# Optimization experiments

Measured on AMD Instinct MI355X. Metric: run time of the kernel, lower is better.

Reference implementation:

```python
import jax, jax.numpy as jnp
import numpy as np

DT = 0.15
DX = 1.0
NUM_STEPS = 4
EPS = 1e-6


def smooth3(m, axis):
    # 3-tap mean filter with replicate padding (matches F.pad replicate + conv1d ones/3)
    pad = [(0, 0)] * m.ndim
    pad[axis] = (1, 1)
    p = jnp.pad(m, pad, mode='edge')
    n = m.shape[axis]
    s = lambda i: jax.lax.slice_in_dim(p, i, i + n, axis=axis)
    return (s(0) + s(1) + s(2)) / 3.0


def thomas(a, b, c, d):
    # a,b,c: [N, *S] coefficient diagonals; d: [N, *B] rhs, S broadcastable into B.
    # Single fused lax.scan per sweep instead of N python-level scatter steps.
    def fwd(carry, inp):
        cp, dp = carry
        ai, bi, ci, di = inp
        denom = bi - ai * cp + EPS  # first step: cp=0 -> b0 + eps, as in torch
        cn = ci / denom
        dn = (di - ai * dp) / denom
        return (cn, dn), (cn, dn)

    init = (jnp.zeros_like(b[0]), jnp.zeros_like(d[0]))
    _, (cs, ds) = jax.lax.scan(fwd, init, (a, b, c, d))
    cs = cs.at[-1].set(0.0)  # torch leaves c_star[N-1] = 0

    def bwd(xn, inp):
        ci, di = inp
        x = di - ci * xn
        return x, x

    _, xs = jax.lax.scan(bwd, jnp.zeros_like(ds[0]), (cs, ds), reverse=True)
    return xs  # [N, *B]


def _tridiag_coeffs(coeff_smooth, dt):
    coeff = coeff_smooth * dt / (DX ** 2)
    a = -coeff
    c = -coeff
    b = 1.0 + 2.0 * coeff
    b = b.at[..., 0].set(1.0 + coeff[..., 0])
    b = b.at[..., -1].set(1.0 + coeff[..., -1])
    return a, b, c


def diffuse_x(u, alpha, dt):
    # u: [B,C,H,W]; alpha: [C,H,W]; implicit solve along W
    asm = smooth3(alpha, axis=2)
    a, b, c = _tridiag_coeffs(asm, dt)  # [C,H,W], endpoints modified along W
    aT = jnp.moveaxis(a, -1, 0)  # [W,C,H]
    bT = jnp.moveaxis(b, -1, 0)
    cT = jnp.moveaxis(c, -1, 0)
    dT = jnp.moveaxis(u, -1, 0)  # [W,B,C,H]
    x = thomas(aT, bT, cT, dT)
    return jnp.moveaxis(x, 0, -1)


def diffuse_y(u, beta, dt):
    # u: [B,C,H,W]; beta: [C,H,W]; implicit solve along H
    bsm = smooth3(beta, axis=1)  # smoothing along H (torch smooths beta.T along last dim)
    coeff = bsm * dt / (DX ** 2)
    a = -coeff
    c = -coeff
    b = 1.0 + 2.0 * coeff
    b = b.at[:, 0, :].set(1.0 + coeff[:, 0, :])
    b = b.at[:, -1, :].set(1.0 + coeff[:, -1, :])
    aT = jnp.moveaxis(a, 1, 0)  # [H,C,W]
    bT = jnp.moveaxis(b, 1, 0)
    cT = jnp.moveaxis(c, 1, 0)
    dT = jnp.moveaxis(u, 2, 0)  # [H,B,C,W]
    x = thomas(aT, bT, cT, dT)
    return jnp.moveaxis(x, 0, 2)


def setup_inputs() -> dict:
    key = jax.random.key(0)
    ks = jax.random.split(key, 6)
    B, C, S = 16384, 3, 32
    u = jax.random.normal(ks[0], (B, C, S, S), dtype=jnp.float32)
    alpha_base = 1.2 + 0.05 * jax.random.normal(ks[1], (C, S, S), dtype=jnp.float32)
    beta_base = 1.2 + 0.05 * jax.random.normal(ks[2], (C, S, S), dtype=jnp.float32)
    alpha_time_coeff = 0.05 * jax.random.normal(ks[3], (C, S, S), dtype=jnp.float32)
    beta_time_coeff = 0.05 * jax.random.normal(ks[4], (C, S, S), dtype=jnp.float32)
    channel_coupling = 0.1 * jnp.eye(C, dtype=jnp.float32) + 0.01 * jax.random.normal(ks[5], (C, C), dtype=jnp.float32)
    return {"u": u, "alpha_base": alpha_base, "beta_base": beta_base,
            "alpha_time_coeff": alpha_time_coeff, "beta_time_coeff": beta_time_coeff,
            "channel_coupling": channel_coupling}


def reference(u, alpha_base, beta_base, alpha_time_coeff, beta_time_coeff, channel_coupling):
    t = 0.0
    for _ in range(NUM_STEPS):
        alpha = jnp.maximum(alpha_base + alpha_time_coeff * t, EPS)
        beta = jnp.maximum(beta_base + beta_time_coeff * t, EPS)
        u = diffuse_x(u, alpha, DT / 2)  # ADI half-step in x
        u = diffuse_y(u, beta, DT)       # full step in y
        u = diffuse_x(u, alpha, DT / 2)  # half-step in x
        # einsum 'cc,bci->bci' with repeated index = per-channel diagonal scaling
        u = jnp.einsum('cc,bchw->bchw', channel_coupling, u)
        t += DT
    return u
```

## Files before the change

kernel.cpp:

```cpp
#include <hip/hip_runtime.h>

#define EPS 1e-6f
#define NSTEPS 4
#define TPB 256
#define TILES 8
#define PITCH 33
#define TSTRIDE (32 * PITCH)

__global__ void coeff_kernel(const float* __restrict__ ab,
                             const float* __restrict__ atc,
                             const float* __restrict__ bb,
                             const float* __restrict__ btc,
                             float4* __restrict__ PX,
                             float4* __restrict__ PY)
{
    int tid = blockIdx.x * blockDim.x + threadIdx.x;
    if (tid >= 768) return;
    int lane = tid & 31;
    int rest = tid >> 5;
    int c    = rest % 3;
    int s    = (rest / 3) & 3;
    int dir  = rest / 12;
    float t  = 0.15f * (float)s;

    float A[32];
    float dt;
    if (dir == 0) {
        int h = lane;
        const float* pa = ab  + (c * 32 + h) * 32;
        const float* pt = atc + (c * 32 + h) * 32;
        #pragma unroll
        for (int w = 0; w < 32; w++)
            A[w] = fmaxf(pa[w] + t * pt[w], EPS);
        dt = 0.075f;
    } else {
        int w = lane;
        #pragma unroll
        for (int h = 0; h < 32; h++)
            A[h] = fmaxf(bb[(c * 32 + h) * 32 + w] + t * btc[(c * 32 + h) * 32 + w], EPS);
        dt = 0.15f;
    }

    float S[32];
    #pragma unroll
    for (int i = 0; i < 32; i++) {
        float l = A[(i == 0) ? 0 : i - 1];
        float r = A[(i == 31) ? 31 : i + 1];
        S[i] = (l + A[i] + r) / 3.0f;
    }

    float4* dst = (dir == 0 ? PX : PY) + ((s * 3 + c) * 32) * 32 + lane;
    float cp = 0.0f;
    for (int i = 0; i < 32; i++) {
        float co = S[i] * dt;
        float a  = -co;
        float b  = (i == 0 || i == 31) ? (1.0f + co) : (1.0f + 2.0f * co);
        float cc = -co;
        float denom = (b - a * cp) + EPS;
        float inv = 1.0f / denom;
        float cs  = cc / denom;
        if (i == 31) cs = 0.0f;
        dst[i * 32] = make_float4(a, inv, cs, 0.0f);
        cp = cs;
    }
}

__global__ __launch_bounds__(TPB, 2)
void diffuse_kernel(const float* __restrict__ u,
                    const float4* __restrict__ PX,
                    const float4* __restrict__ PY,
                    const float* __restrict__ coupling,
                    float* __restrict__ out)
{
    __shared__ float lds[TILES * TSTRIDE];

    const int tid = threadIdx.x;
    const int tl  = tid >> 5;
    const int r   = tid & 31;
    const int nper = gridDim.x / 3;
    const int c    = blockIdx.x / nper;
    const long grp = blockIdx.x % nper;
    const long b0  = grp * TILES + tl;
    const long base = (b0 * 3 + c) << 10;

    float* T = lds + tl * TSTRIDE;

    const float4* src4 = (const float4*)(u + base);
    #pragma unroll
    for (int j = 0; j < 8; j++) {
        float4 v = src4[j * 32 + r];
        int f = (j * 32 + r) * 4;
        int row = f >> 5, col = f & 31;
        float* p = T + row * PITCH + col;
        p[0] = v.x; p[1] = v.y; p[2] = v.z; p[3] = v.w;
    }
    const float kc = coupling[c * 3 + c];
    __syncthreads();

    float val[32];
    float csr[32];

    #pragma unroll 1
    for (int s = 0; s < NSTEPS; s++) {
        const float4* px = PX + (s * 3 + c) * 1024;
        const float4* py = PY + (s * 3 + c) * 1024;

        {
            float dp = 0.0f;
            #pragma unroll
            for (int i = 0; i < 32; i++) {
                float4 p = px[i * 32 + r];
                float d  = (s == 0) ? T[r * PITCH + i] : val[i];
                dp = (d - p.x * dp) * p.y;
                val[i] = dp;
                csr[i] = p.z;
            }
            float x = 0.0f;
            #pragma unroll
            for (int i = 31; i >= 0; i--) {
                x = val[i] - csr[i] * x;
                T[r * PITCH + i] = x;
            }
        }
        __syncthreads();

        {
            float dp = 0.0f;
            #pragma unroll
            for (int i = 0; i < 32; i++) {
                float4 p = py[i * 32 + r];
                float d  = T[i * PITCH + r];
                dp = (d - p.x * dp) * p.y;
                val[i] = dp;
                csr[i] = p.z;
            }
            float x = 0.0f;
            #pragma unroll
            for (int i = 31; i >= 0; i--) {
                x = val[i] - csr[i] * x;
                T[i * PITCH + r] = x;
            }
        }
        __syncthreads();

        {
            float dp = 0.0f;
            #pragma unroll
            for (int i = 0; i < 32; i++) {
                float4 p = px[i * 32 + r];
                float d  = T[r * PITCH + i];
                dp = (d - p.x * dp) * p.y;
                val[i] = dp;
                csr[i] = p.z;
            }
            float x = 0.0f;
            #pragma unroll
            for (int i = 31; i >= 0; i--) {
                x = val[i] - csr[i] * x;
                val[i] = kc * x;
            }
        }
    }

    #pragma unroll
    for (int i = 0; i < 32; i++) T[r * PITCH + i] = val[i];
    __syncthreads();

    float4* dst4 = (float4*)(out + base);
    #pragma unroll
    for (int j = 0; j < 8; j++) {
        int f = (j * 32 + r) * 4;
        int row = f >> 5, col = f & 31;
        float* p = T + row * PITCH + col;
        dst4[j * 32 + r] = make_float4(p[0], p[1], p[2], p[3]);
    }
}

extern "C" void kernel_launch(void* const* d_in, const int* in_sizes, int n_in,
                              void* d_out, int out_size, void* d_ws, size_t ws_size,
                              hipStream_t stream) {
    const float* u   = (const float*)d_in[0];
    const float* ab  = (const float*)d_in[1];
    const float* bb  = (const float*)d_in[2];
    const float* atc = (const float*)d_in[3];
    const float* btc = (const float*)d_in[4];
    const float* cpl = (const float*)d_in[5];
    float* out = (float*)d_out;

    float4* PX = (float4*)d_ws;
    float4* PY = PX + 4 * 3 * 32 * 32;

    coeff_kernel<<<3, 256, 0, stream>>>(ab, atc, bb, btc, PX, PY);

    int B = in_sizes[0] / (3 * 32 * 32);
    int nblocks = (B / TILES) * 3;
    diffuse_kernel<<<nblocks, TPB, 0, stream>>>(u, PX, PY, cpl, out);
}
```

Measured before the change: 565.1 us.

## Split coefficient arrays, drop csr register array, shrink blocks, nontemporal stores

Splits the packed float4 coefficient table into a float2 (a, inv) array and a separate c* array. The backward sweep now reloads c* from global memory instead of keeping a 32-entry register array, which lowers register pressure and allows more waves per SIMD. Blocks shrink to 64 threads with 2 tiles each, launch bounds rise to 4, and output writes use nontemporal stores. In exchange the backward sweep issues extra global/L2 loads, and each block has less work.

```diff
diff --git a/kernel.cpp b/kernel.cpp
--- a/kernel.cpp
+++ b/kernel.cpp
@@ -2,17 +2,21 @@
 
 #define EPS 1e-6f
 #define NSTEPS 4
-#define TPB 256
-#define TILES 8
+#define TPB 64
+#define TILES 2
 #define PITCH 33
 #define TSTRIDE (32 * PITCH)
+
+typedef float floatx4 __attribute__((ext_vector_type(4)));
 
 __global__ void coeff_kernel(const float* __restrict__ ab,
                              const float* __restrict__ atc,
                              const float* __restrict__ bb,
                              const float* __restrict__ btc,
-                             float4* __restrict__ PX,
-                             float4* __restrict__ PY)
+                             float2* __restrict__ FX,
+                             float*  __restrict__ CX,
+                             float2* __restrict__ FY,
+                             float*  __restrict__ CY)
 {
     int tid = blockIdx.x * blockDim.x + threadIdx.x;
     if (tid >= 768) return;
@@ -49,7 +53,8 @@
         S[i] = (l + A[i] + r) / 3.0f;
     }
 
-    float4* dst = (dir == 0 ? PX : PY) + ((s * 3 + c) * 32) * 32 + lane;
+    float2* fdst = (dir == 0 ? FX : FY) + ((s * 3 + c) * 32) * 32 + lane;
+    float*  cdst = (dir == 0 ? CX : CY) + ((s * 3 + c) * 32) * 32 + lane;
     float cp = 0.0f;
     for (int i = 0; i < 32; i++) {
         float co = S[i] * dt;
@@ -60,15 +65,18 @@
         float inv = 1.0f / denom;
         float cs  = cc / denom;
         if (i == 31) cs = 0.0f;
-        dst[i * 32] = make_float4(a, inv, cs, 0.0f);
+        fdst[i * 32] = make_float2(a, inv);
+        cdst[i * 32] = cs;
         cp = cs;
     }
 }
 
-__global__ __launch_bounds__(TPB, 2)
+__global__ __launch_bounds__(TPB, 4)
 void diffuse_kernel(const float* __restrict__ u,
-                    const float4* __restrict__ PX,
-                    const float4* __restrict__ PY,
+                    const float2* __restrict__ FX,
+                    const float*  __restrict__ CX,
+                    const float2* __restrict__ FY,
+                    const float*  __restrict__ CY,
                     const float* __restrict__ coupling,
                     float* __restrict__ out)
 {
@@ -98,27 +106,27 @@
     __syncthreads();
 
     float val[32];
-    float csr[32];
 
     #pragma unroll 1
     for (int s = 0; s < NSTEPS; s++) {
-        const float4* px = PX + (s * 3 + c) * 1024;
-        const float4* py = PY + (s * 3 + c) * 1024;
+        const float2* fx = FX + (s * 3 + c) * 1024;
+        const float*  cx = CX + (s * 3 + c) * 1024;
+        const float2* fy = FY + (s * 3 + c) * 1024;
+        const float*  cy = CY + (s * 3 + c) * 1024;
 
         {
             float dp = 0.0f;
             #pragma unroll
             for (int i = 0; i < 32; i++) {
-                float4 p = px[i * 32 + r];
+                float2 p = fx[i * 32 + r];
                 float d  = (s == 0) ? T[r * PITCH + i] : val[i];
                 dp = (d - p.x * dp) * p.y;
                 val[i] = dp;
-                csr[i] = p.z;
             }
             float x = 0.0f;
             #pragma unroll
             for (int i = 31; i >= 0; i--) {
-                x = val[i] - csr[i] * x;
+                x = val[i] - cx[i * 32 + r] * x;
                 T[r * PITCH + i] = x;
             }
         }
@@ -128,16 +136,15 @@
             float dp = 0.0f;
             #pragma unroll
             for (int i = 0; i < 32; i++) {
-                float4 p = py[i * 32 + r];
+                float2 p = fy[i * 32 + r];
                 float d  = T[i * PITCH + r];
                 dp = (d - p.x * dp) * p.y;
                 val[i] = dp;
-                csr[i] = p.z;
             }
             float x = 0.0f;
             #pragma unroll
             for (int i = 31; i >= 0; i--) {
-                x = val[i] - csr[i] * x;
+                x = val[i] - cy[i * 32 + r] * x;
                 T[i * PITCH + r] = x;
             }
         }
@@ -147,16 +154,15 @@
             float dp = 0.0f;
             #pragma unroll
             for (int i = 0; i < 32; i++) {
-                float4 p = px[i * 32 + r];
+                float2 p = fx[i * 32 + r];
                 float d  = T[r * PITCH + i];
                 dp = (d - p.x * dp) * p.y;
                 val[i] = dp;
-                csr[i] = p.z;
             }
             float x = 0.0f;
             #pragma unroll
             for (int i = 31; i >= 0; i--) {
-                x = val[i] - csr[i] * x;
+                x = val[i] - cx[i * 32 + r] * x;
                 val[i] = kc * x;
             }
         }
@@ -166,13 +172,14 @@
     for (int i = 0; i < 32; i++) T[r * PITCH + i] = val[i];
     __syncthreads();
 
-    float4* dst4 = (float4*)(out + base);
+    floatx4* dst4 = (floatx4*)(out + base);
     #pragma unroll
     for (int j = 0; j < 8; j++) {
         int f = (j * 32 + r) * 4;
         int row = f >> 5, col = f & 31;
         float* p = T + row * PITCH + col;
-        dst4[j * 32 + r] = make_float4(p[0], p[1], p[2], p[3]);
+        floatx4 v = { p[0], p[1], p[2], p[3] };
+        __builtin_nontemporal_store(v, &dst4[j * 32 + r]);
     }
 }
 
@@ -187,12 +194,15 @@
     const float* cpl = (const float*)d_in[5];
     float* out = (float*)d_out;
 
-    float4* PX = (float4*)d_ws;
-    float4* PY = PX + 4 * 3 * 32 * 32;
-
-    coeff_kernel<<<3, 256, 0, stream>>>(ab, atc, bb, btc, PX, PY);
+    const int NC = 4 * 3 * 32 * 32;
+    float2* FX = (float2*)d_ws;
+    float*  CX = (float*)(FX + NC);
+    float2* FY = (float2*)(CX + NC);
+    float*  CY = (float*)(FY + NC);
+
+    coeff_kernel<<<3, 256, 0, stream>>>(ab, atc, bb, btc, FX, CX, FY, CY);
 
     int B = in_sizes[0] / (3 * 32 * 32);
     int nblocks = (B / TILES) * 3;
-    diffuse_kernel<<<nblocks, TPB, 0, stream>>>(u, PX, PY, cpl, out);
+    diffuse_kernel<<<nblocks, TPB, 0, stream>>>(u, FX, CX, FY, CY, cpl, out);
 }
```

Measured after the change: 684.6 us. 1.21x slower.
